# Performance work log

Hardware: AMD Instinct MI355X
Metric: run time of the kernel (lower is better)

## Reference

```python
import jax, jax.numpy as jnp
import numpy as np

BETA = 0.01  # soft-threshold level (init kwarg)
EPS = 1e-12


def vector_to_toeplitz(v):
    # v: [2N-1] complex generator; T[i, j] = v[N-1 + i - j], shape [N, N]
    n = (v.shape[0] + 1) // 2
    ii = jnp.arange(n)[:, None]
    jj = jnp.arange(n)[None, :]
    return v[(n - 1) + ii - jj]


def soft_thresh(z, beta):
    # complex soft-threshold (proximal op of beta*||.||_1):
    # z * max(|z| - beta, 0) / |z|
    mag = jnp.abs(z)
    scale = jnp.maximum(mag - beta, 0.0) / jnp.maximum(mag, EPS)
    return z * scale.astype(z.real.dtype)


def setup_inputs() -> dict:
    key = jax.random.key(0)
    ks = jax.random.split(key, 8)
    N, M, B = 1024, 256, 1024
    d = jnp.float32
    return {
        "v_re": jax.random.normal(ks[0], (2 * N - 1,), d),
        "v_im": jax.random.normal(ks[1], (2 * N - 1,), d),
        "W2_re": jax.random.normal(ks[2], (N, M), d) / np.sqrt(M),
        "W2_im": jax.random.normal(ks[3], (N, M), d) / np.sqrt(M),
        "x_re": jax.random.normal(ks[4], (N, B), d),
        "x_im": jax.random.normal(ks[5], (N, B), d),
        "y_re": jax.random.normal(ks[6], (M, B), d),
        "y_im": jax.random.normal(ks[7], (M, B), d),
    }


def reference(v_re, v_im, W2_re, W2_im, x_re, x_im, y_re, y_im):
    v = jax.lax.complex(v_re, v_im)      # [2N-1]
    W2 = jax.lax.complex(W2_re, W2_im)   # [N, M] (= A^H)
    x = jax.lax.complex(x_re, x_im)      # [N, B]
    y = jax.lax.complex(y_re, y_im)      # [M, B]
    W1 = vector_to_toeplitz(v)           # [N, N] Toeplitz
    # tpm(W1, x) + W2 @ y, then complex soft-threshold
    z = soft_thresh(W1 @ x + W2 @ y, BETA)  # [N, B]
    return z
```

## Files before the change

kernel.cpp:

```cpp
#include <hip/hip_runtime.h>
#include <hip/hip_fp16.h>
#include <cstdint>
#include <cstddef>


#define K_DIM 2560
#define BETA_F 0.01f
#define EPS_F  1e-12f

typedef __attribute__((ext_vector_type(8))) _Float16 half8;
typedef __attribute__((ext_vector_type(4))) _Float16 half4;
typedef __attribute__((ext_vector_type(4))) float   floatx4;

__device__ alignas(16) _Float16 g_Ap[1024 * K_DIM];
__device__ alignas(16) _Float16 g_Bt[2048 * K_DIM];

__global__ __launch_bounds__(256) void build_all(
    const float* __restrict__ v_re, const float* __restrict__ v_im,
    const float* __restrict__ W2_re, const float* __restrict__ W2_im,
    const float* __restrict__ x_re, const float* __restrict__ x_im,
    const float* __restrict__ y_re, const float* __restrict__ y_im)
{
    const int bx = blockIdx.x;
    if (bx < 1280) {
        int t = bx * 256 + threadIdx.x;
        int i  = t / 320;
        int c  = t - i * 320;
        int kp = c * 8;
        half8 h;
        if (kp < 1024) {
#pragma unroll
            for (int j = 0; j < 8; ++j) h[j] = (_Float16)v_re[1023 + i - kp - j];
        } else if (kp < 1280) {
            const float* s = W2_re + i * 256 + (kp - 1024);
#pragma unroll
            for (int j = 0; j < 8; ++j) h[j] = (_Float16)s[j];
        } else if (kp < 2304) {
            int k2 = kp - 1280;
#pragma unroll
            for (int j = 0; j < 8; ++j) h[j] = (_Float16)v_im[1023 + i - k2 - j];
        } else {
            const float* s = W2_im + i * 256 + (kp - 2304);
#pragma unroll
            for (int j = 0; j < 8; ++j) h[j] = (_Float16)s[j];
        }
        *reinterpret_cast<half8*>(g_Ap + (size_t)i * K_DIM + kp) = h;
        return;
    }
    __shared__ float lre[32][33];
    __shared__ float lim[32][33];
    int idx = bx - 1280;
    int bk  = idx % 40;
    int by  = idx / 40;
    const float* sre = (bk < 32) ? x_re : y_re;
    const float* sim = (bk < 32) ? x_im : y_im;
    int kb   = (bk < 32) ? bk : (bk - 32);
    int koff = (bk < 32) ? 0 : 1024;
    int k0 = kb * 32;
    int n0 = by * 32;
    int tid = threadIdx.x;
    int tx = tid & 31, ty = tid >> 5;
#pragma unroll
    for (int s = 0; s < 4; ++s) {
        int kk = ty + 8 * s;
        lre[kk][tx] = sre[(size_t)(k0 + kk) * 1024 + n0 + tx];
        lim[kk][tx] = sim[(size_t)(k0 + kk) * 1024 + n0 + tx];
    }
    __syncthreads();
    int lane_n = tid >> 3;
    int kq     = (tid & 7) * 4;
    half4 hre, him, hmim;
#pragma unroll
    for (int j = 0; j < 4; ++j) {
        float re = lre[kq + j][lane_n];
        float im = lim[kq + j][lane_n];
        hre[j]  = (_Float16)re;
        him[j]  = (_Float16)im;
        hmim[j] = (_Float16)(-im);
    }
    int n = n0 + lane_n;
    size_t kk2 = (size_t)koff + k0 + kq;
    _Float16* r0 = g_Bt + (size_t)(2 * n)     * K_DIM;
    _Float16* r1 = g_Bt + (size_t)(2 * n + 1) * K_DIM;
    *reinterpret_cast<half4*>(r0 + kk2)        = hre;
    *reinterpret_cast<half4*>(r0 + kk2 + 1280) = hmim;
    *reinterpret_cast<half4*>(r1 + kk2)        = him;
    *reinterpret_cast<half4*>(r1 + kk2 + 1280) = hre;
}

__global__ __launch_bounds__(256, 2) void gemm_fused(float* __restrict__ out,
                                                     int out_n)
{
    __shared__ __align__(16) _Float16 As[2 * 4 * 64 * 32];
    __shared__ __align__(16) _Float16 Bs[2 * 4 * 64 * 32];

    const int tid  = threadIdx.x;
    const int lane = tid & 63;
    const int w    = tid >> 6;
    const int wm   = w >> 1;
    const int wn   = w & 1;

    const int bid = blockIdx.x;
    const int xcd = bid & 7;
    const int t   = bid >> 3;
    const int mi0 = ((xcd & 1) * 8 + (t & 7)) * 64;
    const int ni0 = ((xcd >> 1) * 8 + (t >> 3)) * 64;

    floatx4 acc[2][2];
#pragma unroll
    for (int a = 0; a < 2; ++a)
#pragma unroll
        for (int b = 0; b < 2; ++b) acc[a][b] = (floatx4)0.0f;

    const int rS = tid >> 2;
    const int jS = tid & 3;
    const int s0 = ((rS & 15) >> 1) & 3;
    char* asW = (char*)As + rS * 64 + ((jS ^ s0) * 16);
    char* bsW = (char*)Bs + rS * 64 + ((jS ^ s0) * 16);
    const _Float16* gA = g_Ap + (size_t)(mi0 + rS) * K_DIM + jS * 8;
    const _Float16* gB = g_Bt + (size_t)(ni0 + rS) * K_DIM + jS * 8;

    const int rowA = lane & 15;
    const int q    = lane >> 4;
    const int coff = (q ^ ((rowA >> 1) & 3)) * 16;

    const int NIT = K_DIM / 128;

    half8 sA[2][4], sB[2][4];

    {
        half8 tA[4], tB[4];
#pragma unroll
        for (int ks = 0; ks < 4; ++ks) {
            tA[ks] = *reinterpret_cast<const half8*>(gA + ks * 32);
            tB[ks] = *reinterpret_cast<const half8*>(gB + ks * 32);
        }
#pragma unroll
        for (int ks = 0; ks < 4; ++ks) {
            sA[1][ks] = *reinterpret_cast<const half8*>(gA + 128 + ks * 32);
            sB[1][ks] = *reinterpret_cast<const half8*>(gB + 128 + ks * 32);
        }
#pragma unroll
        for (int ks = 0; ks < 4; ++ks) {
            *reinterpret_cast<half8*>(asW + ks * 4096) = tA[ks];
            *reinterpret_cast<half8*>(bsW + ks * 4096) = tB[ks];
        }
    }
    __syncthreads();

#pragma unroll 2
    for (int kt = 0; kt < NIT; ++kt) {
        const int cur = kt & 1;
        const int nxt = cur ^ 1;
        if (kt + 2 < NIT) {
            const _Float16* ga = gA + (size_t)(kt + 2) * 128;
            const _Float16* gb = gB + (size_t)(kt + 2) * 128;
#pragma unroll
            for (int ks = 0; ks < 4; ++ks) {
                sA[cur][ks] = *reinterpret_cast<const half8*>(ga + ks * 32);
                sB[cur][ks] = *reinterpret_cast<const half8*>(gb + ks * 32);
            }
        }
        const char* Ab = (const char*)As + cur * 16384;
        const char* Bb = (const char*)Bs + cur * 16384;
#pragma unroll
        for (int ks = 0; ks < 4; ++ks) {
            half8 af[2], bf[2];
#pragma unroll
            for (int mi = 0; mi < 2; ++mi) {
                int r = wm * 32 + mi * 16 + rowA;
                af[mi] = *reinterpret_cast<const half8*>(Ab + ks * 4096 + r * 64 + coff);
            }
#pragma unroll
            for (int ni = 0; ni < 2; ++ni) {
                int r = wn * 32 + ni * 16 + rowA;
                bf[ni] = *reinterpret_cast<const half8*>(Bb + ks * 4096 + r * 64 + coff);
            }
#pragma unroll
            for (int mi = 0; mi < 2; ++mi)
#pragma unroll
                for (int ni = 0; ni < 2; ++ni)
                    acc[mi][ni] = __builtin_amdgcn_mfma_f32_16x16x32_f16(
                        af[mi], bf[ni], acc[mi][ni], 0, 0, 0);
        }
        if (kt + 1 < NIT) {
            char* aw = asW + nxt * 16384;
            char* bw = bsW + nxt * 16384;
#pragma unroll
            for (int ks = 0; ks < 4; ++ks) {
                *reinterpret_cast<half8*>(aw + ks * 4096) = sA[nxt][ks];
                *reinterpret_cast<half8*>(bw + ks * 4096) = sB[nxt][ks];
            }
        }
        __syncthreads();
    }

    const int colL  = lane & 15;
    const int rquad = (lane >> 4) * 4;
#pragma unroll
    for (int mi = 0; mi < 2; ++mi)
#pragma unroll
        for (int ni = 0; ni < 2; ++ni)
#pragma unroll
            for (int r = 0; r < 4; ++r) {
                float c = acc[mi][ni][r];
                float p = __shfl_xor(c, 1, 64);
                float mag = sqrtf(c * c + p * p);
                float s = fmaxf(mag - BETA_F, 0.0f) / fmaxf(mag, EPS_F);
                int row = mi0 + wm * 32 + mi * 16 + rquad + r;
                int col = ni0 + wn * 32 + ni * 16 + colL;
                if ((col & 1) == 0) {
                    size_t idx = (size_t)row * 1024 + (col >> 1);
                    if (idx < (size_t)out_n) out[idx] = c * s;
                }
            }
}

extern "C" void kernel_launch(void* const* d_in, const int* in_sizes, int n_in,
                              void* d_out, int out_size, void* d_ws, size_t ws_size,
                              hipStream_t stream) {
    (void)d_ws; (void)ws_size; (void)in_sizes; (void)n_in;
    const float* v_re  = (const float*)d_in[0];
    const float* v_im  = (const float*)d_in[1];
    const float* W2_re = (const float*)d_in[2];
    const float* W2_im = (const float*)d_in[3];
    const float* x_re  = (const float*)d_in[4];
    const float* x_im  = (const float*)d_in[5];
    const float* y_re  = (const float*)d_in[6];
    const float* y_im  = (const float*)d_in[7];
    float* out = (float*)d_out;

    build_all<<<2560, 256, 0, stream>>>(v_re, v_im, W2_re, W2_im,
                                        x_re, x_im, y_re, y_im);
    gemm_fused<<<512, 256, 0, stream>>>(out, out_size);
}
```

Before: 107.2 us.

## Use direct global-to-LDS loads in GEMM and vectorize transpose loads in build

The GEMM main loop stops staging tiles through registers and instead issues global_load_lds instructions that write 16-byte chunks straight into shared memory. The XOR swizzle moves from the LDS write address to the global read address, so the existing swizzled fragment reads still line up. Prefetch depth drops from two tiles in flight to one, which cuts register pressure and VGPR-to-LDS store traffic but may expose more load latency. The build kernel's transpose stage also switches to float4 global loads.

```diff
diff --git a/kernel.cpp b/kernel.cpp
--- a/kernel.cpp
+++ b/kernel.cpp
@@ -59,12 +59,18 @@
     int k0 = kb * 32;
     int n0 = by * 32;
     int tid = threadIdx.x;
-    int tx = tid & 31, ty = tid >> 5;
-#pragma unroll
-    for (int s = 0; s < 4; ++s) {
-        int kk = ty + 8 * s;
-        lre[kk][tx] = sre[(size_t)(k0 + kk) * 1024 + n0 + tx];
-        lim[kk][tx] = sim[(size_t)(k0 + kk) * 1024 + n0 + tx];
+    {
+        int kk  = tid >> 3;
+        int tx4 = (tid & 7) * 4;
+        const floatx4 re4 = *reinterpret_cast<const floatx4*>(
+            sre + (size_t)(k0 + kk) * 1024 + n0 + tx4);
+        const floatx4 im4 = *reinterpret_cast<const floatx4*>(
+            sim + (size_t)(k0 + kk) * 1024 + n0 + tx4);
+#pragma unroll
+        for (int j = 0; j < 4; ++j) {
+            lre[kk][tx4 + j] = re4[j];
+            lim[kk][tx4 + j] = im4[j];
+        }
     }
     __syncthreads();
     int lane_n = tid >> 3;
@@ -115,10 +121,10 @@
     const int rS = tid >> 2;
     const int jS = tid & 3;
     const int s0 = ((rS & 15) >> 1) & 3;
-    char* asW = (char*)As + rS * 64 + ((jS ^ s0) * 16);
-    char* bsW = (char*)Bs + rS * 64 + ((jS ^ s0) * 16);
-    const _Float16* gA = g_Ap + (size_t)(mi0 + rS) * K_DIM + jS * 8;
-    const _Float16* gB = g_Bt + (size_t)(ni0 + rS) * K_DIM + jS * 8;
+    const _Float16* gA = g_Ap + (size_t)(mi0 + rS) * K_DIM + (jS ^ s0) * 8;
+    const _Float16* gB = g_Bt + (size_t)(ni0 + rS) * K_DIM + (jS ^ s0) * 8;
+    char* asD = (char*)As + w * 1024;
+    char* bsD = (char*)Bs + w * 1024;
 
     const int rowA = lane & 15;
     const int q    = lane >> 4;
@@ -126,41 +132,31 @@
 
     const int NIT = K_DIM / 128;
 
-    half8 sA[2][4], sB[2][4];
-
-    {
-        half8 tA[4], tB[4];
+    auto stage = [&](int buf, int kt) {
+        const _Float16* ga = gA + (size_t)kt * 128;
+        const _Float16* gb = gB + (size_t)kt * 128;
+        char* ad = asD + buf * 16384;
+        char* bd = bsD + buf * 16384;
 #pragma unroll
         for (int ks = 0; ks < 4; ++ks) {
-            tA[ks] = *reinterpret_cast<const half8*>(gA + ks * 32);
-            tB[ks] = *reinterpret_cast<const half8*>(gB + ks * 32);
-        }
-#pragma unroll
-        for (int ks = 0; ks < 4; ++ks) {
-            sA[1][ks] = *reinterpret_cast<const half8*>(gA + 128 + ks * 32);
-            sB[1][ks] = *reinterpret_cast<const half8*>(gB + 128 + ks * 32);
-        }
-#pragma unroll
-        for (int ks = 0; ks < 4; ++ks) {
-            *reinterpret_cast<half8*>(asW + ks * 4096) = tA[ks];
-            *reinterpret_cast<half8*>(bsW + ks * 4096) = tB[ks];
-        }
-    }
+            __builtin_amdgcn_global_load_lds(
+                (const __attribute__((address_space(1))) void*)(ga + ks * 32),
+                (__attribute__((address_space(3))) void*)(ad + ks * 4096),
+                16, 0, 0);
+            __builtin_amdgcn_global_load_lds(
+                (const __attribute__((address_space(1))) void*)(gb + ks * 32),
+                (__attribute__((address_space(3))) void*)(bd + ks * 4096),
+                16, 0, 0);
+        }
+    };
+
+    stage(0, 0);
     __syncthreads();
 
 #pragma unroll 2
     for (int kt = 0; kt < NIT; ++kt) {
         const int cur = kt & 1;
-        const int nxt = cur ^ 1;
-        if (kt + 2 < NIT) {
-            const _Float16* ga = gA + (size_t)(kt + 2) * 128;
-            const _Float16* gb = gB + (size_t)(kt + 2) * 128;
-#pragma unroll
-            for (int ks = 0; ks < 4; ++ks) {
-                sA[cur][ks] = *reinterpret_cast<const half8*>(ga + ks * 32);
-                sB[cur][ks] = *reinterpret_cast<const half8*>(gb + ks * 32);
-            }
-        }
+        if (kt + 1 < NIT) stage(cur ^ 1, kt + 1);
         const char* Ab = (const char*)As + cur * 16384;
         const char* Bb = (const char*)Bs + cur * 16384;
 #pragma unroll
@@ -182,15 +178,6 @@
                 for (int ni = 0; ni < 2; ++ni)
                     acc[mi][ni] = __builtin_amdgcn_mfma_f32_16x16x32_f16(
                         af[mi], bf[ni], acc[mi][ni], 0, 0, 0);
-        }
-        if (kt + 1 < NIT) {
-            char* aw = asW + nxt * 16384;
-            char* bw = bsW + nxt * 16384;
-#pragma unroll
-            for (int ks = 0; ks < 4; ++ks) {
-                *reinterpret_cast<half8*>(aw + ks * 4096) = sA[nxt][ks];
-                *reinterpret_cast<half8*>(bw + ks * 4096) = sB[nxt][ks];
-            }
         }
         __syncthreads();
     }
```

Result: slower. 116.4 us (+8.6%).

## Split K across waves in GEMM with LDS reduction, vectorize build loads

Applied to the files above, without the earlier changes.

The GEMM changes from a 2x2 wave layout, where each wave computes a 32x32 output quadrant over all K, to a split-K layout. Each wave now owns one 32-wide K slice of every tile and computes the full 64x64 output. After the main loop the waves write partial accumulators to LDS, then each wave reduces one 16-row strip and applies the soft-threshold. This is meant to cut LDS fragment reads per MFMA and give longer MFMA chains. The cost is 16 accumulators per thread, more register pressure at 2 blocks per CU, and an extra LDS reduction pass. The build kernel also switches its x/y loads to float4 vector loads.

```diff
diff --git a/kernel.cpp b/kernel.cpp
--- a/kernel.cpp
+++ b/kernel.cpp
@@ -59,12 +59,18 @@
     int k0 = kb * 32;
     int n0 = by * 32;
     int tid = threadIdx.x;
-    int tx = tid & 31, ty = tid >> 5;
-#pragma unroll
-    for (int s = 0; s < 4; ++s) {
-        int kk = ty + 8 * s;
-        lre[kk][tx] = sre[(size_t)(k0 + kk) * 1024 + n0 + tx];
-        lim[kk][tx] = sim[(size_t)(k0 + kk) * 1024 + n0 + tx];
+    {
+        int kk  = tid >> 3;
+        int tx4 = (tid & 7) * 4;
+        const floatx4 re4 = *reinterpret_cast<const floatx4*>(
+            sre + (size_t)(k0 + kk) * 1024 + n0 + tx4);
+        const floatx4 im4 = *reinterpret_cast<const floatx4*>(
+            sim + (size_t)(k0 + kk) * 1024 + n0 + tx4);
+#pragma unroll
+        for (int j = 0; j < 4; ++j) {
+            lre[kk][tx4 + j] = re4[j];
+            lim[kk][tx4 + j] = im4[j];
+        }
     }
     __syncthreads();
     int lane_n = tid >> 3;
@@ -91,14 +97,11 @@
 __global__ __launch_bounds__(256, 2) void gemm_fused(float* __restrict__ out,
                                                      int out_n)
 {
-    __shared__ __align__(16) _Float16 As[2 * 4 * 64 * 32];
-    __shared__ __align__(16) _Float16 Bs[2 * 4 * 64 * 32];
+    __shared__ __align__(16) char smem[65536];
 
     const int tid  = threadIdx.x;
     const int lane = tid & 63;
     const int w    = tid >> 6;
-    const int wm   = w >> 1;
-    const int wn   = w & 1;
 
     const int bid = blockIdx.x;
     const int xcd = bid & 7;
@@ -106,17 +109,17 @@
     const int mi0 = ((xcd & 1) * 8 + (t & 7)) * 64;
     const int ni0 = ((xcd >> 1) * 8 + (t >> 3)) * 64;
 
-    floatx4 acc[2][2];
-#pragma unroll
-    for (int a = 0; a < 2; ++a)
-#pragma unroll
-        for (int b = 0; b < 2; ++b) acc[a][b] = (floatx4)0.0f;
+    floatx4 acc[4][4];
+#pragma unroll
+    for (int a = 0; a < 4; ++a)
+#pragma unroll
+        for (int b = 0; b < 4; ++b) acc[a][b] = (floatx4)0.0f;
 
     const int rS = tid >> 2;
     const int jS = tid & 3;
     const int s0 = ((rS & 15) >> 1) & 3;
-    char* asW = (char*)As + rS * 64 + ((jS ^ s0) * 16);
-    char* bsW = (char*)Bs + rS * 64 + ((jS ^ s0) * 16);
+    char* asW = smem         + rS * 64 + ((jS ^ s0) * 16);
+    char* bsW = smem + 32768 + rS * 64 + ((jS ^ s0) * 16);
     const _Float16* gA = g_Ap + (size_t)(mi0 + rS) * K_DIM + jS * 8;
     const _Float16* gB = g_Bt + (size_t)(ni0 + rS) * K_DIM + jS * 8;
 
@@ -161,28 +164,21 @@
                 sB[cur][ks] = *reinterpret_cast<const half8*>(gb + ks * 32);
             }
         }
-        const char* Ab = (const char*)As + cur * 16384;
-        const char* Bb = (const char*)Bs + cur * 16384;
-#pragma unroll
-        for (int ks = 0; ks < 4; ++ks) {
-            half8 af[2], bf[2];
-#pragma unroll
-            for (int mi = 0; mi < 2; ++mi) {
-                int r = wm * 32 + mi * 16 + rowA;
-                af[mi] = *reinterpret_cast<const half8*>(Ab + ks * 4096 + r * 64 + coff);
-            }
-#pragma unroll
-            for (int ni = 0; ni < 2; ++ni) {
-                int r = wn * 32 + ni * 16 + rowA;
-                bf[ni] = *reinterpret_cast<const half8*>(Bb + ks * 4096 + r * 64 + coff);
-            }
-#pragma unroll
-            for (int mi = 0; mi < 2; ++mi)
-#pragma unroll
-                for (int ni = 0; ni < 2; ++ni)
-                    acc[mi][ni] = __builtin_amdgcn_mfma_f32_16x16x32_f16(
-                        af[mi], bf[ni], acc[mi][ni], 0, 0, 0);
-        }
+        const char* Ab = smem         + cur * 16384 + w * 4096;
+        const char* Bb = smem + 32768 + cur * 16384 + w * 4096;
+        half8 af[4], bf[4];
+#pragma unroll
+        for (int mi = 0; mi < 4; ++mi)
+            af[mi] = *reinterpret_cast<const half8*>(Ab + (mi * 16 + rowA) * 64 + coff);
+#pragma unroll
+        for (int ni = 0; ni < 4; ++ni)
+            bf[ni] = *reinterpret_cast<const half8*>(Bb + (ni * 16 + rowA) * 64 + coff);
+#pragma unroll
+        for (int mi = 0; mi < 4; ++mi)
+#pragma unroll
+            for (int ni = 0; ni < 4; ++ni)
+                acc[mi][ni] = __builtin_amdgcn_mfma_f32_16x16x32_f16(
+                    af[mi], bf[ni], acc[mi][ni], 0, 0, 0);
         if (kt + 1 < NIT) {
             char* aw = asW + nxt * 16384;
             char* bw = bsW + nxt * 16384;
@@ -195,25 +191,36 @@
         __syncthreads();
     }
 
+    float* L = (float*)smem;
+#pragma unroll
+    for (int mi = 0; mi < 4; ++mi)
+#pragma unroll
+        for (int ni = 0; ni < 4; ++ni)
+#pragma unroll
+            for (int r = 0; r < 4; ++r)
+                L[(((w * 4 + mi) * 4 + ni) * 4 + r) * 64 + lane] = acc[mi][ni][r];
+    __syncthreads();
+
     const int colL  = lane & 15;
     const int rquad = (lane >> 4) * 4;
 #pragma unroll
-    for (int mi = 0; mi < 2; ++mi)
-#pragma unroll
-        for (int ni = 0; ni < 2; ++ni)
-#pragma unroll
-            for (int r = 0; r < 4; ++r) {
-                float c = acc[mi][ni][r];
-                float p = __shfl_xor(c, 1, 64);
-                float mag = sqrtf(c * c + p * p);
-                float s = fmaxf(mag - BETA_F, 0.0f) / fmaxf(mag, EPS_F);
-                int row = mi0 + wm * 32 + mi * 16 + rquad + r;
-                int col = ni0 + wn * 32 + ni * 16 + colL;
-                if ((col & 1) == 0) {
-                    size_t idx = (size_t)row * 1024 + (col >> 1);
-                    if (idx < (size_t)out_n) out[idx] = c * s;
-                }
+    for (int ni = 0; ni < 4; ++ni)
+#pragma unroll
+        for (int r = 0; r < 4; ++r) {
+            float c = 0.0f;
+#pragma unroll
+            for (int wp = 0; wp < 4; ++wp)
+                c += L[(((wp * 4 + w) * 4 + ni) * 4 + r) * 64 + lane];
+            float p = __shfl_xor(c, 1, 64);
+            float mag = sqrtf(c * c + p * p);
+            float s = fmaxf(mag - BETA_F, 0.0f) / fmaxf(mag, EPS_F);
+            int row = mi0 + w * 16 + rquad + r;
+            int col = ni0 + ni * 16 + colL;
+            if ((col & 1) == 0) {
+                size_t idx = (size_t)row * 1024 + (col >> 1);
+                if (idx < (size_t)out_n) out[idx] = c * s;
             }
+        }
 }
 
 extern "C" void kernel_launch(void* const* d_in, const int* in_sizes, int n_in,
```

Measured after the change: 108.4 us. No clear change (+1.1%).

## Replace Toeplitz GEMM with FFT-based circulant convolution plus small W2·y GEMM

Applied to the files above, without the earlier changes.

The Toeplitz product W1@x is now computed as a length-2048 FFT convolution per batch column in shared memory, with the generator spectrum precomputed once by a single block. The fp16 MFMA GEMM is kept only for the small W2@y term (K=512), and a separate combine kernel adds both parts, transposes the conv result and applies the soft-threshold. This removes the O(N^2 B) Toeplitz matmul, but adds extra fp32 intermediate buffers, a transpose pass, more kernel launches, and a radix-2 FFT bound by shared memory and barriers.

```diff
diff --git a/kernel.cpp b/kernel.cpp
--- a/kernel.cpp
+++ b/kernel.cpp
@@ -4,7 +4,6 @@
 #include <cstddef>
 
 
-#define K_DIM 2560
 #define BETA_F 0.01f
 #define EPS_F  1e-12f
 
@@ -12,8 +11,12 @@
 typedef __attribute__((ext_vector_type(4))) _Float16 half4;
 typedef __attribute__((ext_vector_type(4))) float   floatx4;
 
-__device__ alignas(16) _Float16 g_Ap[1024 * K_DIM];
-__device__ alignas(16) _Float16 g_Bt[2048 * K_DIM];
+__device__ alignas(16) _Float16 g_A2[1024 * 512];
+__device__ alignas(16) _Float16 g_B2t[2048 * 512];
+__device__ alignas(16) float2   g_xT[1024 * 1024];
+__device__ alignas(16) float2   g_V[2048];
+__device__ alignas(16) float2   g_convT[1024 * 1024];
+__device__ alignas(16) float2   g_w2y[1024 * 1024];
 
 __global__ __launch_bounds__(256) void build_all(
     const float* __restrict__ v_re, const float* __restrict__ v_im,
@@ -21,75 +24,150 @@
     const float* __restrict__ x_re, const float* __restrict__ x_im,
     const float* __restrict__ y_re, const float* __restrict__ y_im)
 {
-    const int bx = blockIdx.x;
-    if (bx < 1280) {
-        int t = bx * 256 + threadIdx.x;
-        int i  = t / 320;
-        int c  = t - i * 320;
-        int kp = c * 8;
+    __shared__ __align__(16) char sbuf[24576];
+    const int bx  = blockIdx.x;
+    const int tid = threadIdx.x;
+
+    if (bx < 256) {
+        int t  = bx * 256 + tid;
+        int i  = t >> 6;
+        int kp = (t & 63) * 8;
         half8 h;
-        if (kp < 1024) {
-#pragma unroll
-            for (int j = 0; j < 8; ++j) h[j] = (_Float16)v_re[1023 + i - kp - j];
-        } else if (kp < 1280) {
-            const float* s = W2_re + i * 256 + (kp - 1024);
+        if (kp < 256) {
+            const float* s = W2_re + i * 256 + kp;
 #pragma unroll
             for (int j = 0; j < 8; ++j) h[j] = (_Float16)s[j];
-        } else if (kp < 2304) {
-            int k2 = kp - 1280;
-#pragma unroll
-            for (int j = 0; j < 8; ++j) h[j] = (_Float16)v_im[1023 + i - k2 - j];
         } else {
-            const float* s = W2_im + i * 256 + (kp - 2304);
+            const float* s = W2_im + i * 256 + (kp - 256);
 #pragma unroll
             for (int j = 0; j < 8; ++j) h[j] = (_Float16)s[j];
         }
-        *reinterpret_cast<half8*>(g_Ap + (size_t)i * K_DIM + kp) = h;
+        *reinterpret_cast<half8*>(g_A2 + (size_t)i * 512 + kp) = h;
         return;
     }
-    __shared__ float lre[32][33];
-    __shared__ float lim[32][33];
-    int idx = bx - 1280;
-    int bk  = idx % 40;
-    int by  = idx / 40;
-    const float* sre = (bk < 32) ? x_re : y_re;
-    const float* sim = (bk < 32) ? x_im : y_im;
-    int kb   = (bk < 32) ? bk : (bk - 32);
-    int koff = (bk < 32) ? 0 : 1024;
-    int k0 = kb * 32;
-    int n0 = by * 32;
-    int tid = threadIdx.x;
-    int tx = tid & 31, ty = tid >> 5;
-#pragma unroll
-    for (int s = 0; s < 4; ++s) {
-        int kk = ty + 8 * s;
-        lre[kk][tx] = sre[(size_t)(k0 + kk) * 1024 + n0 + tx];
-        lim[kk][tx] = sim[(size_t)(k0 + kk) * 1024 + n0 + tx];
+    if (bx < 512) {
+        float (*lre)[33] = (float(*)[33])sbuf;
+        float (*lim)[33] = (float(*)[33])(sbuf + 4224);
+        int idx = bx - 256;
+        int bk  = idx & 7;
+        int by  = idx >> 3;
+        int k0  = bk * 32;
+        int n0  = by * 32;
+        {
+            int kk  = tid >> 3;
+            int tx4 = (tid & 7) * 4;
+            const floatx4 re4 = *reinterpret_cast<const floatx4*>(
+                y_re + (size_t)(k0 + kk) * 1024 + n0 + tx4);
+            const floatx4 im4 = *reinterpret_cast<const floatx4*>(
+                y_im + (size_t)(k0 + kk) * 1024 + n0 + tx4);
+#pragma unroll
+            for (int j = 0; j < 4; ++j) {
+                lre[kk][tx4 + j] = re4[j];
+                lim[kk][tx4 + j] = im4[j];
+            }
+        }
+        __syncthreads();
+        int lane_n = tid >> 3;
+        int kq     = (tid & 7) * 4;
+        half4 hre, him, hmim;
+#pragma unroll
+        for (int j = 0; j < 4; ++j) {
+            float re = lre[kq + j][lane_n];
+            float im = lim[kq + j][lane_n];
+            hre[j]  = (_Float16)re;
+            him[j]  = (_Float16)im;
+            hmim[j] = (_Float16)(-im);
+        }
+        int n = n0 + lane_n;
+        _Float16* r0 = g_B2t + (size_t)(2 * n)     * 512;
+        _Float16* r1 = g_B2t + (size_t)(2 * n + 1) * 512;
+        *reinterpret_cast<half4*>(r0 + k0 + kq)       = hre;
+        *reinterpret_cast<half4*>(r0 + 256 + k0 + kq) = hmim;
+        *reinterpret_cast<half4*>(r1 + k0 + kq)       = him;
+        *reinterpret_cast<half4*>(r1 + 256 + k0 + kq) = hre;
+        return;
+    }
+    if (bx < 1536) {
+        float (*lre)[33] = (float(*)[33])sbuf;
+        float (*lim)[33] = (float(*)[33])(sbuf + 4224);
+        int idx = bx - 512;
+        int n0  = (idx >> 5) * 32;
+        int b0  = (idx & 31) * 32;
+        {
+            int kk  = tid >> 3;
+            int tx4 = (tid & 7) * 4;
+            const floatx4 re4 = *reinterpret_cast<const floatx4*>(
+                x_re + (size_t)(n0 + kk) * 1024 + b0 + tx4);
+            const floatx4 im4 = *reinterpret_cast<const floatx4*>(
+                x_im + (size_t)(n0 + kk) * 1024 + b0 + tx4);
+#pragma unroll
+            for (int j = 0; j < 4; ++j) {
+                lre[kk][tx4 + j] = re4[j];
+                lim[kk][tx4 + j] = im4[j];
+            }
+        }
+        __syncthreads();
+        int bb  = tid >> 3;
+        int nn4 = (tid & 7) * 4;
+        float2* dst = g_xT + (size_t)(b0 + bb) * 1024 + n0 + nn4;
+        floatx4 w0, w1;
+        w0[0] = lre[nn4 + 0][bb]; w0[1] = lim[nn4 + 0][bb];
+        w0[2] = lre[nn4 + 1][bb]; w0[3] = lim[nn4 + 1][bb];
+        w1[0] = lre[nn4 + 2][bb]; w1[1] = lim[nn4 + 2][bb];
+        w1[2] = lre[nn4 + 3][bb]; w1[3] = lim[nn4 + 3][bb];
+        *reinterpret_cast<floatx4*>(dst)     = w0;
+        *reinterpret_cast<floatx4*>(dst + 2) = w1;
+        return;
+    }
+    float2* du = (float2*)sbuf;
+    float*  twr = (float*)(sbuf + 16384);
+    float*  twi = (float*)(sbuf + 20480);
+#pragma unroll
+    for (int r = 0; r < 4; ++r) {
+        int k = tid + 256 * r;
+        float ang = (float)k * 3.0679615757712823e-3f;
+        float s, c;
+        __sincosf(ang, &s, &c);
+        twr[k] = c; twi[k] = -s;
+    }
+#pragma unroll
+    for (int r = 0; r < 8; ++r) {
+        int k = tid + 256 * r;
+        float2 val;
+        if (k < 1024)      { val.x = v_re[1023 + k]; val.y = v_im[1023 + k]; }
+        else if (k == 1024){ val.x = 0.f; val.y = 0.f; }
+        else               { val.x = v_re[k - 1025]; val.y = v_im[k - 1025]; }
+        du[k] = val;
+    }
+    for (int s = 0; s < 11; ++s) {
+        int lh = 10 - s, h = 1 << lh;
+        __syncthreads();
+#pragma unroll
+        for (int r = 0; r < 4; ++r) {
+            int i  = tid + 256 * r;
+            int j  = i & (h - 1);
+            int i0 = ((i >> lh) << (lh + 1)) | j;
+            int i1 = i0 + h;
+            float2 a = du[i0], b = du[i1];
+            float dx = a.x - b.x, dy = a.y - b.y;
+            int ti = j << s;
+            float wr = twr[ti], wi = twi[ti];
+            float2 s0; s0.x = a.x + b.x; s0.y = a.y + b.y;
+            float2 d0; d0.x = dx * wr - dy * wi; d0.y = dx * wi + dy * wr;
+            du[i0] = s0; du[i1] = d0;
+        }
     }
     __syncthreads();
-    int lane_n = tid >> 3;
-    int kq     = (tid & 7) * 4;
-    half4 hre, him, hmim;
-#pragma unroll
-    for (int j = 0; j < 4; ++j) {
-        float re = lre[kq + j][lane_n];
-        float im = lim[kq + j][lane_n];
-        hre[j]  = (_Float16)re;
-        him[j]  = (_Float16)im;
-        hmim[j] = (_Float16)(-im);
-    }
-    int n = n0 + lane_n;
-    size_t kk2 = (size_t)koff + k0 + kq;
-    _Float16* r0 = g_Bt + (size_t)(2 * n)     * K_DIM;
-    _Float16* r1 = g_Bt + (size_t)(2 * n + 1) * K_DIM;
-    *reinterpret_cast<half4*>(r0 + kk2)        = hre;
-    *reinterpret_cast<half4*>(r0 + kk2 + 1280) = hmim;
-    *reinterpret_cast<half4*>(r1 + kk2)        = him;
-    *reinterpret_cast<half4*>(r1 + kk2 + 1280) = hre;
+#pragma unroll
+    for (int r = 0; r < 8; ++r) {
+        int k = tid + 256 * r;
+        float2 v = du[k];
+        v.x *= (1.0f / 2048.0f); v.y *= (1.0f / 2048.0f);
+        g_V[k] = v;
+    }
 }
 
-__global__ __launch_bounds__(256, 2) void gemm_fused(float* __restrict__ out,
-                                                     int out_n)
+__global__ __launch_bounds__(256, 2) void gemm_w2y()
 {
     __shared__ __align__(16) _Float16 As[2 * 4 * 64 * 32];
     __shared__ __align__(16) _Float16 Bs[2 * 4 * 64 * 32];
@@ -117,17 +195,16 @@
     const int s0 = ((rS & 15) >> 1) & 3;
     char* asW = (char*)As + rS * 64 + ((jS ^ s0) * 16);
     char* bsW = (char*)Bs + rS * 64 + ((jS ^ s0) * 16);
-    const _Float16* gA = g_Ap + (size_t)(mi0 + rS) * K_DIM + jS * 8;
-    const _Float16* gB = g_Bt + (size_t)(ni0 + rS) * K_DIM + jS * 8;
+    const _Float16* gA = g_A2  + (size_t)(mi0 + rS) * 512 + jS * 8;
+    const _Float16* gB = g_B2t + (size_t)(ni0 + rS) * 512 + jS * 8;
 
     const int rowA = lane & 15;
     const int q    = lane >> 4;
     const int coff = (q ^ ((rowA >> 1) & 3)) * 16;
 
-    const int NIT = K_DIM / 128;
+    const int NIT = 512 / 128;
 
     half8 sA[2][4], sB[2][4];
-
     {
         half8 tA[4], tB[4];
 #pragma unroll
@@ -205,15 +282,127 @@
             for (int r = 0; r < 4; ++r) {
                 float c = acc[mi][ni][r];
                 float p = __shfl_xor(c, 1, 64);
-                float mag = sqrtf(c * c + p * p);
-                float s = fmaxf(mag - BETA_F, 0.0f) / fmaxf(mag, EPS_F);
-                int row = mi0 + wm * 32 + mi * 16 + rquad + r;
-                int col = ni0 + wn * 32 + ni * 16 + colL;
-                if ((col & 1) == 0) {
-                    size_t idx = (size_t)row * 1024 + (col >> 1);
-                    if (idx < (size_t)out_n) out[idx] = c * s;
+                if (!(colL & 1)) {
+                    int row = mi0 + wm * 32 + mi * 16 + rquad + r;
+                    int col = ni0 + wn * 32 + ni * 16 + colL;
+                    float2 v; v.x = c; v.y = p;
+                    g_w2y[(size_t)row * 1024 + (col >> 1)] = v;
                 }
             }
+}
+
+__global__ __launch_bounds__(256, 2) void fft_conv()
+{
+    __shared__ float2 dat[2][2048];
+    __shared__ float  twr[1024];
+    __shared__ float  twi[1024];
+
+    const int tid = threadIdx.x;
+    const int c   = tid >> 7;
+    const int tl  = tid & 127;
+    const int b0  = blockIdx.x * 2;
+
+#pragma unroll
+    for (int r = 0; r < 4; ++r) {
+        int k = tid + 256 * r;
+        float ang = (float)k * 3.0679615757712823e-3f;
+        float s, cc;
+        __sincosf(ang, &s, &cc);
+        twr[k] = cc; twi[k] = -s;
+    }
+    const float2* src = g_xT + (size_t)(b0 + c) * 1024;
+#pragma unroll
+    for (int r = 0; r < 8; ++r) {
+        int n = tl + 128 * r;
+        dat[c][n] = src[n];
+    }
+#pragma unroll
+    for (int r = 8; r < 16; ++r) {
+        int n = tl + 128 * r;
+        float2 z; z.x = 0.f; z.y = 0.f;
+        dat[c][n] = z;
+    }
+
+    for (int s = 0; s < 11; ++s) {
+        int lh = 10 - s, h = 1 << lh;
+        __syncthreads();
+#pragma unroll
+        for (int r = 0; r < 8; ++r) {
+            int i  = tl + 128 * r;
+            int j  = i & (h - 1);
+            int i0 = ((i >> lh) << (lh + 1)) | j;
+            int i1 = i0 + h;
+            float2 a = dat[c][i0], b = dat[c][i1];
+            float dx = a.x - b.x, dy = a.y - b.y;
+            int ti = j << s;
+            float wr = twr[ti], wi = twi[ti];
+            float2 s0; s0.x = a.x + b.x; s0.y = a.y + b.y;
+            float2 d0; d0.x = dx * wr - dy * wi; d0.y = dx * wi + dy * wr;
+            dat[c][i0] = s0; dat[c][i1] = d0;
+        }
+    }
+    __syncthreads();
+#pragma unroll
+    for (int r = 0; r < 16; ++r) {
+        int k = tl + 128 * r;
+        float2 a = dat[c][k], v = g_V[k];
+        float2 m; m.x = a.x * v.x - a.y * v.y; m.y = a.x * v.y + a.y * v.x;
+        dat[c][k] = m;
+    }
+    for (int ss = 0; ss < 11; ++ss) {
+        int h = 1 << ss;
+        __syncthreads();
+#pragma unroll
+        for (int r = 0; r < 8; ++r) {
+            int i  = tl + 128 * r;
+            int j  = i & (h - 1);
+            int i0 = ((i >> ss) << (ss + 1)) | j;
+            int i1 = i0 + h;
+            int ti = j << (10 - ss);
+            float wr = twr[ti], wi = twi[ti];
+            float2 a = dat[c][i0], b = dat[c][i1];
+            float2 bt; bt.x = b.x * wr + b.y * wi; bt.y = b.y * wr - b.x * wi;
+            float2 p0; p0.x = a.x + bt.x; p0.y = a.y + bt.y;
+            float2 p1; p1.x = a.x - bt.x; p1.y = a.y - bt.y;
+            dat[c][i0] = p0; dat[c][i1] = p1;
+        }
+    }
+    __syncthreads();
+    float2* dst = g_convT + (size_t)(b0 + c) * 1024;
+#pragma unroll
+    for (int r = 0; r < 8; ++r) {
+        int n = tl + 128 * r;
+        dst[n] = dat[c][n];
+    }
+}
+
+__global__ __launch_bounds__(256) void combine(float* __restrict__ out, int out_n)
+{
+    __shared__ float2 cvl[32][33];
+    const int tid = threadIdx.x;
+    const int bx  = blockIdx.x;
+    const int i0  = (bx >> 5) * 32;
+    const int b0  = (bx & 31) * 32;
+#pragma unroll
+    for (int r = 0; r < 4; ++r) {
+        int rr = r * 8 + (tid >> 5);
+        int cc = tid & 31;
+        cvl[rr][cc] = g_convT[(size_t)(b0 + rr) * 1024 + i0 + cc];
+    }
+    __syncthreads();
+#pragma unroll
+    for (int r = 0; r < 4; ++r) {
+        int ii = r * 8 + (tid >> 5);
+        int bb = tid & 31;
+        float2 w2 = g_w2y[(size_t)(i0 + ii) * 1024 + b0 + bb];
+        float2 cv = cvl[bb][ii];
+        float re = w2.x + cv.x;
+        float im = w2.y + cv.y;
+        float mag = sqrtf(re * re + im * im);
+        float s = fmaxf(mag - BETA_F, 0.0f) / fmaxf(mag, EPS_F);
+        size_t o = (size_t)(i0 + ii) * 1024 + b0 + bb;
+        if (o < (size_t)out_n) out[o] = re * s;
+    }
 }
 
 extern "C" void kernel_launch(void* const* d_in, const int* in_sizes, int n_in,
@@ -230,7 +419,9 @@
     const float* y_im  = (const float*)d_in[7];
     float* out = (float*)d_out;
 
-    build_all<<<2560, 256, 0, stream>>>(v_re, v_im, W2_re, W2_im,
+    build_all<<<1537, 256, 0, stream>>>(v_re, v_im, W2_re, W2_im,
                                         x_re, x_im, y_re, y_im);
-    gemm_fused<<<512, 256, 0, stream>>>(out, out_size);
+    gemm_w2y<<<512, 256, 0, stream>>>();
+    fft_conv<<<512, 256, 0, stream>>>();
+    combine<<<1024, 256, 0, stream>>>(out, out_size);
 }
```

Result: slower. 141.2 us (+31.8%).
